# Performance work log

Measured on AMD Instinct MI355X. Metric: run time of the kernel, lower is better.

## Reference

```python
import jax, jax.numpy as jnp
import numpy as np

N, H, W, C = 4, 64, 64, 256
G, K = 8, 3
GC = C // G
P = K * K
PAD = 1
BN_EPS = 1e-3  # ultralytics Conv uses BatchNorm2d(eps=0.001)


def setup_inputs() -> dict:
    key = jax.random.key(0)
    ks = jax.random.split(key, 8)
    return {
        "x": jax.random.normal(ks[0], (N, H, W, C), jnp.float32),
        # depthwise conv weight (OIHW with I=1, feature_group_count=C)
        "dw_w": jax.random.normal(ks[1], (C, 1, K, K), jnp.float32) * 0.1,
        "bn_gamma": jnp.ones((C,), jnp.float32),
        "bn_beta": jnp.zeros((C,), jnp.float32),
        "bn_mean": jnp.zeros((C,), jnp.float32),
        "bn_var": jnp.ones((C,), jnp.float32),
        # offset/mask heads are zero-init in torch; use small random weights so
        # sampling locations are nontrivial but stay near the kernel grid
        "W_off": jax.random.normal(ks[2], (C, G * P * 2), jnp.float32) * 0.01,
        "b_off": jnp.zeros((G * P * 2,), jnp.float32),
        "W_mask": jax.random.normal(ks[3], (C, G * P), jnp.float32) * 0.01,
        "b_mask": jnp.zeros((G * P,), jnp.float32),
        "W_in": jax.random.normal(ks[4], (C, C), jnp.float32) / np.sqrt(C).astype(np.float32),
        "b_in": jnp.zeros((C,), jnp.float32),
        "W_out": jax.random.normal(ks[5], (C, C), jnp.float32) / np.sqrt(C).astype(np.float32),
        "b_out": jnp.zeros((C,), jnp.float32),
    }


def _grid_sample(img, grid):
    # img: (B, gc, Hi, Wi); grid: (B, L, P, 2) in [-1,1], (x,y) order.
    # Matches torch grid_sample(mode='bilinear', padding_mode='zeros', align_corners=False).
    B, gc, Hi, Wi = img.shape
    x = (grid[..., 0] + 1.0) * (Wi * 0.5) - 0.5
    y = (grid[..., 1] + 1.0) * (Hi * 0.5) - 0.5
    x0 = jnp.floor(x).astype(jnp.int32)
    y0 = jnp.floor(y).astype(jnp.int32)
    tx = x - x0
    ty = y - y0
    flat = img.reshape(B, gc, Hi * Wi)
    L, Pp = grid.shape[1], grid.shape[2]

    def tap(xi, yi, w):
        valid = (xi >= 0) & (xi < Wi) & (yi >= 0) & (yi < Hi)
        idx = jnp.clip(yi, 0, Hi - 1) * Wi + jnp.clip(xi, 0, Wi - 1)
        v = jnp.take_along_axis(flat, idx.reshape(B, 1, L * Pp), axis=2)
        v = v.reshape(B, gc, L, Pp)
        return v * (w * valid)[:, None]

    return (tap(x0, y0, (1 - tx) * (1 - ty))
            + tap(x0 + 1, y0, tx * (1 - ty))
            + tap(x0, y0 + 1, (1 - tx) * ty)
            + tap(x0 + 1, y0 + 1, tx * ty))


def _dcnv3_core(xp, offset, mask):
    # xp: (N,H,W,C) projected input; offset: (N,H,W,G*P*2); mask: (N,H,W,G*P)
    xpad = jnp.pad(xp, ((0, 0), (PAD, PAD), (PAD, PAD), (0, 0)))
    Hi, Wi = H + 2 * PAD, W + 2 * PAD
    # reference points on the padded grid, normalized to [0,1]
    start = (K - 1) // 2 + 0.5  # dilation=1, stride=1
    ref_y = (start + jnp.arange(H, dtype=jnp.float32)) / Hi
    ref_x = (start + jnp.arange(W, dtype=jnp.float32)) / Wi
    ref = jnp.stack(jnp.broadcast_arrays(ref_x[None, :], ref_y[:, None]), -1)  # (H,W,2) (x,y)
    # kernel dilation grid; torch meshgrid('ij') over (kw,kh) -> point p = iw*K + ih
    xv = jnp.arange(K, dtype=jnp.float32) - ((K - 1) // 2)
    gx, gy = jnp.meshgrid(xv / Wi, xv / Hi, indexing='ij')
    kgrid = jnp.stack([gx, gy], -1).reshape(P, 2)  # identical per group
    off = offset.reshape(N, H, W, G, P, 2) / jnp.array([Wi, Hi], jnp.float32)
    loc = ref[None, :, :, None, None, :] + kgrid[None, None, None, None] + off  # (N,H,W,G,P,2)
    sg = 2.0 * loc - 1.0
    # regroup channels-last input to (N*G, GC, Hi, Wi); channel c = g*GC + d
    img = xpad.reshape(N, Hi * Wi, G, GC).transpose(0, 2, 3, 1).reshape(N * G, GC, Hi, Wi)
    sgrid = sg.reshape(N, H * W, G, P, 2).transpose(0, 2, 1, 3, 4).reshape(N * G, H * W, P, 2)
    samp = _grid_sample(img, sgrid)  # (N*G, GC, L, P)
    m = mask.reshape(N, H * W, G, P).transpose(0, 2, 1, 3).reshape(N * G, 1, H * W, P)
    out = (samp * m).sum(-1)  # (N*G, GC, L)
    return out.reshape(N, C, H * W).transpose(0, 2, 1).reshape(N, H, W, C)


def reference(x, dw_w, bn_gamma, bn_beta, bn_mean, bn_var, W_off, b_off,
              W_mask, b_mask, W_in, b_in, W_out, b_out):
    x_proj = x @ W_in + b_in
    # depthwise 3x3 conv + BN (eval) + SiLU (ultralytics Conv)
    xc = x.transpose(0, 3, 1, 2)
    y = jax.lax.conv_general_dilated(
        xc, dw_w, (1, 1), ((PAD, PAD), (PAD, PAD)),
        feature_group_count=C, dimension_numbers=('NCHW', 'OIHW', 'NCHW'))
    scale = bn_gamma / jnp.sqrt(bn_var + BN_EPS)
    y = (y - bn_mean[None, :, None, None]) * scale[None, :, None, None] + bn_beta[None, :, None, None]
    y = y * jax.nn.sigmoid(y)
    x1 = y.transpose(0, 2, 3, 1)  # (N,H,W,C)
    offset = x1 @ W_off + b_off
    mlog = (x1 @ W_mask + b_mask).reshape(N, H, W, G, P)
    mask = jax.nn.softmax(mlog, axis=-1).reshape(N, H, W, G * P)
    out = _dcnv3_core(x_proj, offset, mask)
    return out @ W_out + b_out
```

## Files before the change

kernel.cpp:

```cpp
#include <hip/hip_runtime.h>
#include <math.h>

#define NPIX 16384
#define CC 256
#define OFFW 144
#define MSKW 72

typedef unsigned short ushortT;
typedef __attribute__((ext_vector_type(4))) float f32x4;
typedef __attribute__((ext_vector_type(8))) __bf16 bf16x8;
typedef __attribute__((ext_vector_type(8))) unsigned short u16x8;
typedef __attribute__((ext_vector_type(4))) unsigned int u32x4;

__device__ __forceinline__ float bf2f(ushortT u) {
    union { unsigned u; float f; } x; x.u = ((unsigned)u) << 16; return x.f;
}
__device__ __forceinline__ ushortT f2bf(float f) {
    __bf16 h = (__bf16)f;
    ushortT u;
    __builtin_memcpy(&u, &h, 2);
    return u;
}
__device__ __forceinline__ float bflo(unsigned u) { return __uint_as_float(u << 16); }
__device__ __forceinline__ float bfhi(unsigned u) { return __uint_as_float(u & 0xFFFF0000u); }

typedef __attribute__((address_space(3))) char lds_char;
typedef __attribute__((address_space(1))) char glb_char;
__device__ __forceinline__ void gload_lds16(const void* g, void* l) {
    __builtin_amdgcn_global_load_lds((const glb_char*)g, (lds_char*)l, 16, 0, 0);
}

__global__ __launch_bounds__(256) void k_wt(
    const float* __restrict__ W_in, const float* __restrict__ W_out,
    const float* __restrict__ W_off, const float* __restrict__ W_mask,
    const float* __restrict__ b_in, const float* __restrict__ b_out,
    const float* __restrict__ b_off, const float* __restrict__ b_mask,
    ushortT* __restrict__ Wt, float* __restrict__ biasb)
{
    const int idx = blockIdx.x * 256 + threadIdx.x;
    const int slot = idx >> 16;
    const int rem = idx & 65535;
    const int n = rem >> 8, k = rem & 255;
    float v;
    if (slot == 0)      v = W_in[k * 256 + n];
    else if (slot == 1) v = W_out[k * 256 + n];
    else {
        const int g = n >> 5, r = n & 31;
        if (r < 18)      v = W_off[k * OFFW + g * 18 + r];
        else if (r < 27) v = W_mask[k * MSKW + g * 9 + (r - 18)];
        else             v = 0.f;
    }
    Wt[idx] = f2bf(v);
    if (n == 0) {
        float b;
        if (slot == 0)      b = b_in[k];
        else if (slot == 1) b = b_out[k];
        else {
            const int g = k >> 5, r = k & 31;
            b = (r < 18) ? b_off[g * 18 + r] : (r < 27 ? b_mask[g * 9 + (r - 18)] : 0.f);
        }
        biasb[slot * 256 + k] = b;
    }
}

__global__ __launch_bounds__(512, 4) void k_fused_in(
    const float* __restrict__ x, const float* __restrict__ dw_w,
    const float* __restrict__ bn_gamma, const float* __restrict__ bn_beta,
    const float* __restrict__ bn_mean, const float* __restrict__ bn_var,
    const ushortT* __restrict__ Wt, const float* __restrict__ biasb,
    ushortT* __restrict__ xpb, ushortT* __restrict__ omb)
{
    __shared__ __align__(16) ushortT xA[32 * 256];
    __shared__ __align__(16) ushortT x1s[32 * 256];
    const int tid = threadIdx.x;
    const int b0 = blockIdx.x;
    const int lb = (b0 & 7) * 64 + (b0 >> 3);
    const int base = lb * 32;
    const int n = base >> 12, h = (base >> 6) & 63, bw0 = base & 63;

    const int lane = tid & 63, wave = tid >> 6;
    const int gemm = wave >> 2, wc = wave & 3;
    const ushortT* Bt = Wt + (gemm ? 2 * 65536 : 0);

    {
        const int c = tid & 255, half = tid >> 8;
        float wreg[9];
        #pragma unroll
        for (int k = 0; k < 9; ++k) wreg[k] = dw_w[c * 9 + k];
        const float scale = bn_gamma[c] * rsqrtf(bn_var[c] + 1e-3f);
        const float mean = bn_mean[c], beta = bn_beta[c];
        const bool hv0 = h >= 1, hv2 = h <= 62;
        const float* r0 = x + ((size_t)(n * 64 + h - 1) * 64) * 256 + c;
        const float* r1 = x + ((size_t)(n * 64 + h) * 64) * 256 + c;
        const float* r2 = x + ((size_t)(n * 64 + h + 1) * 64) * 256 + c;
        const int w0 = bw0 + half * 16;
        float a0, a1, a2, e0, e1, e2;
        if (w0 - 1 >= 0) {
            a0 = hv0 ? r0[(w0 - 1) * 256] : 0.f;
            a1 = r1[(w0 - 1) * 256];
            a2 = hv2 ? r2[(w0 - 1) * 256] : 0.f;
        } else { a0 = a1 = a2 = 0.f; }
        e0 = hv0 ? r0[w0 * 256] : 0.f;
        e1 = r1[w0 * 256];
        e2 = hv2 ? r2[w0 * 256] : 0.f;
        #pragma unroll
        for (int i = 0; i < 16; ++i) {
            const int w = w0 + i;
            float d0, d1, d2;
            if (w + 1 < 64) {
                d0 = hv0 ? r0[(w + 1) * 256] : 0.f;
                d1 = r1[(w + 1) * 256];
                d2 = hv2 ? r2[(w + 1) * 256] : 0.f;
            } else { d0 = d1 = d2 = 0.f; }
            const float accv = a0 * wreg[0] + e0 * wreg[1] + d0 * wreg[2]
                             + a1 * wreg[3] + e1 * wreg[4] + d1 * wreg[5]
                             + a2 * wreg[6] + e2 * wreg[7] + d2 * wreg[8];
            const float yv = (accv - mean) * scale + beta;
            const float s = yv * __builtin_amdgcn_rcpf(1.f + __expf(-yv));
            const int row = half * 16 + i;
            const int sb = (row * 512 + c * 2) ^ ((row & 15) << 4);
            *(ushortT*)((char*)x1s + sb) = f2bf(s);
            *(ushortT*)((char*)xA + sb) = f2bf(e1);
            a0 = e0; a1 = e1; a2 = e2;
            e0 = d0; e1 = d1; e2 = d2;
        }
    }

    bf16x8 bbp[4];
    #pragma unroll
    for (int nn = 0; nn < 4; ++nn) {
        const int ncol = wc * 64 + nn * 16 + (lane & 15);
        bbp[nn] = *(const bf16x8*)(Bt + (size_t)ncol * 256 + (lane >> 4) * 8);
    }
    __syncthreads();

    const ushortT* As = gemm ? x1s : xA;
    const float* bias = biasb + (gemm ? 512 : 0);
    ushortT* Cout = gemm ? omb : xpb;

    f32x4 acc[2][4];
    #pragma unroll
    for (int m = 0; m < 2; ++m)
        #pragma unroll
        for (int nn = 0; nn < 4; ++nn) acc[m][nn] = (f32x4){0.f, 0.f, 0.f, 0.f};

    #pragma unroll
    for (int k0 = 0; k0 < 256; k0 += 32) {
        bf16x8 af[2], bb[4];
        #pragma unroll
        for (int nn = 0; nn < 4; ++nn) bb[nn] = bbp[nn];
        if (k0 + 32 < 256) {
            #pragma unroll
            for (int nn = 0; nn < 4; ++nn) {
                const int ncol = wc * 64 + nn * 16 + (lane & 15);
                bbp[nn] = *(const bf16x8*)(Bt + (size_t)ncol * 256 + (k0 + 32) + (lane >> 4) * 8);
            }
        }
        #pragma unroll
        for (int m = 0; m < 2; ++m) {
            const int row = m * 16 + (lane & 15);
            af[m] = *(const bf16x8*)((const char*)As + row * 512 +
                     (((k0 + (lane >> 4) * 8) * 2) ^ ((row & 15) << 4)));
        }
        #pragma unroll
        for (int m = 0; m < 2; ++m)
            #pragma unroll
            for (int nn = 0; nn < 4; ++nn)
                acc[m][nn] = __builtin_amdgcn_mfma_f32_16x16x32_bf16(af[m], bb[nn], acc[m][nn], 0, 0, 0);
    }

    const int rbase = (lane >> 4) * 4, col16 = lane & 15;
    #pragma unroll
    for (int m = 0; m < 2; ++m) {
        #pragma unroll
        for (int nn = 0; nn < 4; ++nn) {
            const int col = wc * 64 + nn * 16 + col16;
            const float bj = bias[col];
            #pragma unroll
            for (int r = 0; r < 4; ++r) {
                const int row = m * 16 + rbase + r;
                Cout[(size_t)(base + row) * 256 + col] = f2bf(acc[m][nn][r] + bj);
            }
        }
    }
}

__global__ __launch_bounds__(256) void k_core(
    const ushortT* __restrict__ omb, const ushortT* __restrict__ xpb,
    ushortT* __restrict__ coreb)
{
    const int tid = threadIdx.x;
    const int b0 = blockIdx.x;
    const int lb = (b0 & 7) * 256 + (b0 >> 3);
    const int base = lb * 8;
    const int n = base >> 12, h = (base >> 6) & 63, w0 = base & 63;

    const int px = tid >> 5, g = (tid >> 2) & 7, o = tid & 3;

    const ushortT* omp = omb + (size_t)(base + px) * 256 + g * 32;
    const u32x4 L0 = *(const u32x4*)(omp);
    const u32x4 L1 = *(const u32x4*)(omp + 8);
    const u32x4 L2 = *(const u32x4*)(omp + 16);
    const u32x4 L3 = *(const u32x4*)(omp + 24);
    unsigned opair[9];
    #pragma unroll
    for (int p = 0; p < 4; ++p) { opair[p] = L0[p]; opair[4 + p] = L1[p]; }
    opair[8] = L2[0];
    float lg[9];
    lg[0] = bflo(L2[1]); lg[1] = bfhi(L2[1]);
    lg[2] = bflo(L2[2]); lg[3] = bfhi(L2[2]);
    lg[4] = bflo(L2[3]); lg[5] = bfhi(L2[3]);
    lg[6] = bflo(L3[0]); lg[7] = bfhi(L3[0]);
    lg[8] = bflo(L3[1]);
    float mx = -1e30f;
    #pragma unroll
    for (int p = 0; p < 9; ++p) mx = fmaxf(mx, lg[p]);
    float sum = 0.f;
    #pragma unroll
    for (int p = 0; p < 9; ++p) sum += __expf(lg[p] - mx);
    const float inv = __builtin_amdgcn_rcpf(sum);

    const ushortT* xn = xpb + (size_t)n * (4096 * 256) + g * 32 + o * 8;
    float acc[8];
    #pragma unroll
    for (int j = 0; j < 8; ++j) acc[j] = 0.f;

    #pragma unroll
    for (int p = 0; p < 9; ++p) {
        const float m = __expf(lg[p] - mx) * inv;
        const float ox = bflo(opair[p]), oy = bfhi(opair[p]);
        const float pxc = (float)(w0 + px + p / 3) + ox;
        const float pyc = (float)(h + p % 3) + oy;
        const float xf = floorf(pxc), yf = floorf(pyc);
        const float tx = pxc - xf, ty = pyc - yf;
        const int x0 = (int)xf - 1, y0 = (int)yf - 1;
        const int x1 = x0 + 1, y1 = y0 + 1;
        const float wx0 = ((unsigned)x0 < 64u) ? (1.f - tx) : 0.f;
        const float wx1 = ((unsigned)x1 < 64u) ? tx : 0.f;
        const float wy0 = ((unsigned)y0 < 64u) ? (1.f - ty) : 0.f;
        const float wy1 = ((unsigned)y1 < 64u) ? ty : 0.f;
        const int cx0 = min(max(x0, 0), 63), cx1 = min(max(x1, 0), 63);
        const int cy0 = min(max(y0, 0), 63), cy1 = min(max(y1, 0), 63);
        const int o00 = (cy0 * 64 + cx0) * 256;
        const int o10 = (cy0 * 64 + cx1) * 256;
        const int o01 = (cy1 * 64 + cx0) * 256;
        const int o11 = (cy1 * 64 + cx1) * 256;
        const float w00 = m * wx0 * wy0, w10 = m * wx1 * wy0;
        const float w01 = m * wx0 * wy1, w11 = m * wx1 * wy1;
        const u32x4 A = *(const u32x4*)(xn + o00);
        const u32x4 B = *(const u32x4*)(xn + o10);
        const u32x4 C = *(const u32x4*)(xn + o01);
        const u32x4 D = *(const u32x4*)(xn + o11);
        #pragma unroll
        for (int i = 0; i < 4; ++i) {
            acc[2 * i]     += w00 * bflo(A[i]) + w10 * bflo(B[i])
                            + w01 * bflo(C[i]) + w11 * bflo(D[i]);
            acc[2 * i + 1] += w00 * bfhi(A[i]) + w10 * bfhi(B[i])
                            + w01 * bfhi(C[i]) + w11 * bfhi(D[i]);
        }
    }
    u16x8 cv;
    #pragma unroll
    for (int j = 0; j < 8; ++j) cv[j] = f2bf(acc[j]);
    *(u16x8*)(coreb + (size_t)(base + px) * 256 + g * 32 + o * 8) = cv;
}

__global__ __launch_bounds__(512) void k_gemm_out(
    const ushortT* __restrict__ A, const ushortT* __restrict__ Bt,
    const float* __restrict__ bias, float* __restrict__ out)
{
    __shared__ __align__(16) ushortT As[32 * 256];
    const int tid = threadIdx.x;
    const int m0 = blockIdx.x * 32;
    const int lane = tid & 63, wave = tid >> 6;

    #pragma unroll
    for (int it = 0; it < 2; ++it) {
        const int i = it * 512 + tid;
        const int row = i >> 5, ch = i & 31;
        const int sch = ch ^ (row & 15);
        gload_lds16(A + (size_t)(m0 + row) * 256 + sch * 8, (char*)As + i * 16);
    }
    bf16x8 bbp[2];
    #pragma unroll
    for (int nn = 0; nn < 2; ++nn) {
        const int ncol = wave * 32 + nn * 16 + (lane & 15);
        bbp[nn] = *(const bf16x8*)(Bt + (size_t)ncol * 256 + (lane >> 4) * 8);
    }
    asm volatile("s_waitcnt vmcnt(0)");
    __syncthreads();

    f32x4 acc[2][2];
    #pragma unroll
    for (int m = 0; m < 2; ++m)
        #pragma unroll
        for (int nn = 0; nn < 2; ++nn) acc[m][nn] = (f32x4){0.f, 0.f, 0.f, 0.f};

    #pragma unroll
    for (int k0 = 0; k0 < 256; k0 += 32) {
        bf16x8 af[2], bb[2];
        #pragma unroll
        for (int nn = 0; nn < 2; ++nn) bb[nn] = bbp[nn];
        if (k0 + 32 < 256) {
            #pragma unroll
            for (int nn = 0; nn < 2; ++nn) {
                const int ncol = wave * 32 + nn * 16 + (lane & 15);
                bbp[nn] = *(const bf16x8*)(Bt + (size_t)ncol * 256 + (k0 + 32) + (lane >> 4) * 8);
            }
        }
        #pragma unroll
        for (int m = 0; m < 2; ++m) {
            const int row = m * 16 + (lane & 15);
            af[m] = *(const bf16x8*)((const char*)As + row * 512 +
                     (((k0 + (lane >> 4) * 8) * 2) ^ ((row & 15) << 4)));
        }
        #pragma unroll
        for (int m = 0; m < 2; ++m)
            #pragma unroll
            for (int nn = 0; nn < 2; ++nn)
                acc[m][nn] = __builtin_amdgcn_mfma_f32_16x16x32_bf16(af[m], bb[nn], acc[m][nn], 0, 0, 0);
    }

    const int rbase = (lane >> 4) * 4, col16 = lane & 15;
    #pragma unroll
    for (int m = 0; m < 2; ++m) {
        #pragma unroll
        for (int nn = 0; nn < 2; ++nn) {
            const int col = wave * 32 + nn * 16 + col16;
            const float bj = bias[col];
            #pragma unroll
            for (int r = 0; r < 4; ++r) {
                const int row = m0 + m * 16 + rbase + r;
                out[(size_t)row * 256 + col] = acc[m][nn][r] + bj;
            }
        }
    }
}

extern "C" void kernel_launch(void* const* d_in, const int* in_sizes, int n_in,
                              void* d_out, int out_size, void* d_ws, size_t ws_size,
                              hipStream_t stream) {
    const float* x        = (const float*)d_in[0];
    const float* dw_w     = (const float*)d_in[1];
    const float* bn_gamma = (const float*)d_in[2];
    const float* bn_beta  = (const float*)d_in[3];
    const float* bn_mean  = (const float*)d_in[4];
    const float* bn_var   = (const float*)d_in[5];
    const float* W_off    = (const float*)d_in[6];
    const float* b_off    = (const float*)d_in[7];
    const float* W_mask   = (const float*)d_in[8];
    const float* b_mask   = (const float*)d_in[9];
    const float* W_in     = (const float*)d_in[10];
    const float* b_in     = (const float*)d_in[11];
    const float* W_out    = (const float*)d_in[12];
    const float* b_out    = (const float*)d_in[13];
    float* out = (float*)d_out;

    char* w = (char*)d_ws;
    ushortT* Wt    = (ushortT*)w;
    float* biasb   = (float*)(w + 393216);
    ushortT* xpb   = (ushortT*)(w + 396288);
    ushortT* omb   = (ushortT*)(w + 396288 + 8388608);
    ushortT* coreb = (ushortT*)(w + 396288 + 2 * 8388608);

    hipLaunchKernelGGL(k_wt, dim3(768), dim3(256), 0, stream,
                       W_in, W_out, W_off, W_mask, b_in, b_out, b_off, b_mask, Wt, biasb);
    hipLaunchKernelGGL(k_fused_in, dim3(512), dim3(512), 0, stream,
                       x, dw_w, bn_gamma, bn_beta, bn_mean, bn_var, Wt, biasb, xpb, omb);
    hipLaunchKernelGGL(k_core, dim3(2048), dim3(256), 0, stream,
                       omb, xpb, coreb);
    hipLaunchKernelGGL(k_gemm_out, dim3(NPIX / 32), dim3(512), 0, stream,
                       coreb, Wt + 65536, biasb + 256, out);
}
```

Measured before the change: 63.88 us.

## Fuse deformable sampling core with output projection GEMM via LDS

Merges the bilinear-sampling core kernel and the output-projection MFMA GEMM into one kernel. Each 512-thread block samples 32 pixels, with each thread now handling 16 channels, and writes the bf16 result into a swizzled LDS tile that feeds the GEMM directly. This removes the global round trip of the intermediate core tensor and one kernel launch. In exchange there are fewer, larger blocks (512 instead of 2048 core blocks) with more registers per thread, which may reduce latency hiding for the gather loads.

```diff
diff --git a/kernel.cpp b/kernel.cpp
--- a/kernel.cpp
+++ b/kernel.cpp
@@ -23,12 +23,6 @@
 }
 __device__ __forceinline__ float bflo(unsigned u) { return __uint_as_float(u << 16); }
 __device__ __forceinline__ float bfhi(unsigned u) { return __uint_as_float(u & 0xFFFF0000u); }
-
-typedef __attribute__((address_space(3))) char lds_char;
-typedef __attribute__((address_space(1))) char glb_char;
-__device__ __forceinline__ void gload_lds16(const void* g, void* l) {
-    __builtin_amdgcn_global_load_lds((const glb_char*)g, (lds_char*)l, 16, 0, 0);
-}
 
 __global__ __launch_bounds__(256) void k_wt(
     const float* __restrict__ W_in, const float* __restrict__ W_out,
@@ -185,116 +179,117 @@
     }
 }
 
-__global__ __launch_bounds__(256) void k_core(
+__global__ __launch_bounds__(512) void k_core_out(
     const ushortT* __restrict__ omb, const ushortT* __restrict__ xpb,
-    ushortT* __restrict__ coreb)
+    const ushortT* __restrict__ Wt1, const float* __restrict__ bias1,
+    float* __restrict__ out)
 {
+    __shared__ __align__(16) ushortT core[32 * 256];
     const int tid = threadIdx.x;
     const int b0 = blockIdx.x;
-    const int lb = (b0 & 7) * 256 + (b0 >> 3);
-    const int base = lb * 8;
+    const int lb = (b0 & 7) * 64 + (b0 >> 3);
+    const int base = lb * 32;
     const int n = base >> 12, h = (base >> 6) & 63, w0 = base & 63;
 
-    const int px = tid >> 5, g = (tid >> 2) & 7, o = tid & 3;
-
-    const ushortT* omp = omb + (size_t)(base + px) * 256 + g * 32;
-    const u32x4 L0 = *(const u32x4*)(omp);
-    const u32x4 L1 = *(const u32x4*)(omp + 8);
-    const u32x4 L2 = *(const u32x4*)(omp + 16);
-    const u32x4 L3 = *(const u32x4*)(omp + 24);
-    unsigned opair[9];
-    #pragma unroll
-    for (int p = 0; p < 4; ++p) { opair[p] = L0[p]; opair[4 + p] = L1[p]; }
-    opair[8] = L2[0];
-    float lg[9];
-    lg[0] = bflo(L2[1]); lg[1] = bfhi(L2[1]);
-    lg[2] = bflo(L2[2]); lg[3] = bfhi(L2[2]);
-    lg[4] = bflo(L2[3]); lg[5] = bfhi(L2[3]);
-    lg[6] = bflo(L3[0]); lg[7] = bfhi(L3[0]);
-    lg[8] = bflo(L3[1]);
-    float mx = -1e30f;
-    #pragma unroll
-    for (int p = 0; p < 9; ++p) mx = fmaxf(mx, lg[p]);
-    float sum = 0.f;
-    #pragma unroll
-    for (int p = 0; p < 9; ++p) sum += __expf(lg[p] - mx);
-    const float inv = __builtin_amdgcn_rcpf(sum);
-
-    const ushortT* xn = xpb + (size_t)n * (4096 * 256) + g * 32 + o * 8;
-    float acc[8];
-    #pragma unroll
-    for (int j = 0; j < 8; ++j) acc[j] = 0.f;
-
-    #pragma unroll
-    for (int p = 0; p < 9; ++p) {
-        const float m = __expf(lg[p] - mx) * inv;
-        const float ox = bflo(opair[p]), oy = bfhi(opair[p]);
-        const float pxc = (float)(w0 + px + p / 3) + ox;
-        const float pyc = (float)(h + p % 3) + oy;
-        const float xf = floorf(pxc), yf = floorf(pyc);
-        const float tx = pxc - xf, ty = pyc - yf;
-        const int x0 = (int)xf - 1, y0 = (int)yf - 1;
-        const int x1 = x0 + 1, y1 = y0 + 1;
-        const float wx0 = ((unsigned)x0 < 64u) ? (1.f - tx) : 0.f;
-        const float wx1 = ((unsigned)x1 < 64u) ? tx : 0.f;
-        const float wy0 = ((unsigned)y0 < 64u) ? (1.f - ty) : 0.f;
-        const float wy1 = ((unsigned)y1 < 64u) ? ty : 0.f;
-        const int cx0 = min(max(x0, 0), 63), cx1 = min(max(x1, 0), 63);
-        const int cy0 = min(max(y0, 0), 63), cy1 = min(max(y1, 0), 63);
-        const int o00 = (cy0 * 64 + cx0) * 256;
-        const int o10 = (cy0 * 64 + cx1) * 256;
-        const int o01 = (cy1 * 64 + cx0) * 256;
-        const int o11 = (cy1 * 64 + cx1) * 256;
-        const float w00 = m * wx0 * wy0, w10 = m * wx1 * wy0;
-        const float w01 = m * wx0 * wy1, w11 = m * wx1 * wy1;
-        const u32x4 A = *(const u32x4*)(xn + o00);
-        const u32x4 B = *(const u32x4*)(xn + o10);
-        const u32x4 C = *(const u32x4*)(xn + o01);
-        const u32x4 D = *(const u32x4*)(xn + o11);
-        #pragma unroll
-        for (int i = 0; i < 4; ++i) {
-            acc[2 * i]     += w00 * bflo(A[i]) + w10 * bflo(B[i])
-                            + w01 * bflo(C[i]) + w11 * bflo(D[i]);
-            acc[2 * i + 1] += w00 * bfhi(A[i]) + w10 * bfhi(B[i])
-                            + w01 * bfhi(C[i]) + w11 * bfhi(D[i]);
-        }
-    }
-    u16x8 cv;
-    #pragma unroll
-    for (int j = 0; j < 8; ++j) cv[j] = f2bf(acc[j]);
-    *(u16x8*)(coreb + (size_t)(base + px) * 256 + g * 32 + o * 8) = cv;
-}
-
-__global__ __launch_bounds__(512) void k_gemm_out(
-    const ushortT* __restrict__ A, const ushortT* __restrict__ Bt,
-    const float* __restrict__ bias, float* __restrict__ out)
-{
-    __shared__ __align__(16) ushortT As[32 * 256];
-    const int tid = threadIdx.x;
-    const int m0 = blockIdx.x * 32;
     const int lane = tid & 63, wave = tid >> 6;
 
-    #pragma unroll
-    for (int it = 0; it < 2; ++it) {
-        const int i = it * 512 + tid;
-        const int row = i >> 5, ch = i & 31;
-        const int sch = ch ^ (row & 15);
-        gload_lds16(A + (size_t)(m0 + row) * 256 + sch * 8, (char*)As + i * 16);
-    }
+    {
+        const int px = tid >> 4, s = tid & 15;
+        const int g = s >> 1, half = s & 1;
+        const int c0 = g * 32 + half * 16;
+
+        const ushortT* omp = omb + (size_t)(base + px) * 256 + g * 32;
+        const u32x4 L0 = *(const u32x4*)(omp);
+        const u32x4 L1 = *(const u32x4*)(omp + 8);
+        const u32x4 L2 = *(const u32x4*)(omp + 16);
+        const u32x4 L3 = *(const u32x4*)(omp + 24);
+        unsigned opair[9];
+        #pragma unroll
+        for (int p = 0; p < 4; ++p) { opair[p] = L0[p]; opair[4 + p] = L1[p]; }
+        opair[8] = L2[0];
+        float lg[9];
+        lg[0] = bflo(L2[1]); lg[1] = bfhi(L2[1]);
+        lg[2] = bflo(L2[2]); lg[3] = bfhi(L2[2]);
+        lg[4] = bflo(L2[3]); lg[5] = bfhi(L2[3]);
+        lg[6] = bflo(L3[0]); lg[7] = bfhi(L3[0]);
+        lg[8] = bflo(L3[1]);
+        float mx = -1e30f;
+        #pragma unroll
+        for (int p = 0; p < 9; ++p) mx = fmaxf(mx, lg[p]);
+        float sum = 0.f;
+        #pragma unroll
+        for (int p = 0; p < 9; ++p) sum += __expf(lg[p] - mx);
+        const float inv = __builtin_amdgcn_rcpf(sum);
+
+        const ushortT* xn = xpb + (size_t)n * (4096 * 256) + c0;
+        float acc[16];
+        #pragma unroll
+        for (int j = 0; j < 16; ++j) acc[j] = 0.f;
+
+        #pragma unroll
+        for (int p = 0; p < 9; ++p) {
+            const float m = __expf(lg[p] - mx) * inv;
+            const float ox = bflo(opair[p]), oy = bfhi(opair[p]);
+            const float pxc = (float)(w0 + px + p / 3) + ox;
+            const float pyc = (float)(h + p % 3) + oy;
+            const float xf = floorf(pxc), yf = floorf(pyc);
+            const float tx = pxc - xf, ty = pyc - yf;
+            const int x0 = (int)xf - 1, y0 = (int)yf - 1;
+            const int x1 = x0 + 1, y1 = y0 + 1;
+            const float wx0 = ((unsigned)x0 < 64u) ? (1.f - tx) : 0.f;
+            const float wx1 = ((unsigned)x1 < 64u) ? tx : 0.f;
+            const float wy0 = ((unsigned)y0 < 64u) ? (1.f - ty) : 0.f;
+            const float wy1 = ((unsigned)y1 < 64u) ? ty : 0.f;
+            const int cx0 = min(max(x0, 0), 63), cx1 = min(max(x1, 0), 63);
+            const int cy0 = min(max(y0, 0), 63), cy1 = min(max(y1, 0), 63);
+            const int o00 = (cy0 * 64 + cx0) * 256;
+            const int o10 = (cy0 * 64 + cx1) * 256;
+            const int o01 = (cy1 * 64 + cx0) * 256;
+            const int o11 = (cy1 * 64 + cx1) * 256;
+            const float w00 = m * wx0 * wy0, w10 = m * wx1 * wy0;
+            const float w01 = m * wx0 * wy1, w11 = m * wx1 * wy1;
+            const u32x4 A0 = *(const u32x4*)(xn + o00);
+            const u32x4 A1 = *(const u32x4*)(xn + o00 + 8);
+            const u32x4 B0 = *(const u32x4*)(xn + o10);
+            const u32x4 B1 = *(const u32x4*)(xn + o10 + 8);
+            const u32x4 C0 = *(const u32x4*)(xn + o01);
+            const u32x4 C1 = *(const u32x4*)(xn + o01 + 8);
+            const u32x4 D0 = *(const u32x4*)(xn + o11);
+            const u32x4 D1 = *(const u32x4*)(xn + o11 + 8);
+            #pragma unroll
+            for (int i = 0; i < 4; ++i) {
+                acc[2 * i]     += w00 * bflo(A0[i]) + w10 * bflo(B0[i])
+                                + w01 * bflo(C0[i]) + w11 * bflo(D0[i]);
+                acc[2 * i + 1] += w00 * bfhi(A0[i]) + w10 * bfhi(B0[i])
+                                + w01 * bfhi(C0[i]) + w11 * bfhi(D0[i]);
+                acc[8 + 2 * i]     += w00 * bflo(A1[i]) + w10 * bflo(B1[i])
+                                    + w01 * bflo(C1[i]) + w11 * bflo(D1[i]);
+                acc[8 + 2 * i + 1] += w00 * bfhi(A1[i]) + w10 * bfhi(B1[i])
+                                    + w01 * bfhi(C1[i]) + w11 * bfhi(D1[i]);
+            }
+        }
+        u16x8 cv0, cv1;
+        #pragma unroll
+        for (int j = 0; j < 8; ++j) { cv0[j] = f2bf(acc[j]); cv1[j] = f2bf(acc[8 + j]); }
+        const int sb0 = (px * 512 + c0 * 2) ^ ((px & 15) << 4);
+        const int sb1 = (px * 512 + c0 * 2 + 16) ^ ((px & 15) << 4);
+        *(u16x8*)((char*)core + sb0) = cv0;
+        *(u16x8*)((char*)core + sb1) = cv1;
+    }
+
     bf16x8 bbp[2];
     #pragma unroll
     for (int nn = 0; nn < 2; ++nn) {
         const int ncol = wave * 32 + nn * 16 + (lane & 15);
-        bbp[nn] = *(const bf16x8*)(Bt + (size_t)ncol * 256 + (lane >> 4) * 8);
-    }
-    asm volatile("s_waitcnt vmcnt(0)");
+        bbp[nn] = *(const bf16x8*)(Wt1 + (size_t)ncol * 256 + (lane >> 4) * 8);
+    }
     __syncthreads();
 
-    f32x4 acc[2][2];
+    f32x4 acc2[2][2];
     #pragma unroll
     for (int m = 0; m < 2; ++m)
         #pragma unroll
-        for (int nn = 0; nn < 2; ++nn) acc[m][nn] = (f32x4){0.f, 0.f, 0.f, 0.f};
+        for (int nn = 0; nn < 2; ++nn) acc2[m][nn] = (f32x4){0.f, 0.f, 0.f, 0.f};
 
     #pragma unroll
     for (int k0 = 0; k0 < 256; k0 += 32) {
@@ -305,20 +300,20 @@
             #pragma unroll
             for (int nn = 0; nn < 2; ++nn) {
                 const int ncol = wave * 32 + nn * 16 + (lane & 15);
-                bbp[nn] = *(const bf16x8*)(Bt + (size_t)ncol * 256 + (k0 + 32) + (lane >> 4) * 8);
+                bbp[nn] = *(const bf16x8*)(Wt1 + (size_t)ncol * 256 + (k0 + 32) + (lane >> 4) * 8);
             }
         }
         #pragma unroll
         for (int m = 0; m < 2; ++m) {
             const int row = m * 16 + (lane & 15);
-            af[m] = *(const bf16x8*)((const char*)As + row * 512 +
+            af[m] = *(const bf16x8*)((const char*)core + row * 512 +
                      (((k0 + (lane >> 4) * 8) * 2) ^ ((row & 15) << 4)));
         }
         #pragma unroll
         for (int m = 0; m < 2; ++m)
             #pragma unroll
             for (int nn = 0; nn < 2; ++nn)
-                acc[m][nn] = __builtin_amdgcn_mfma_f32_16x16x32_bf16(af[m], bb[nn], acc[m][nn], 0, 0, 0);
+                acc2[m][nn] = __builtin_amdgcn_mfma_f32_16x16x32_bf16(af[m], bb[nn], acc2[m][nn], 0, 0, 0);
     }
 
     const int rbase = (lane >> 4) * 4, col16 = lane & 15;
@@ -327,11 +322,11 @@
         #pragma unroll
         for (int nn = 0; nn < 2; ++nn) {
             const int col = wave * 32 + nn * 16 + col16;
-            const float bj = bias[col];
+            const float bj = bias1[col];
             #pragma unroll
             for (int r = 0; r < 4; ++r) {
-                const int row = m0 + m * 16 + rbase + r;
-                out[(size_t)row * 256 + col] = acc[m][nn][r] + bj;
+                const int row = base + m * 16 + rbase + r;
+                out[(size_t)row * 256 + col] = acc2[m][nn][r] + bj;
             }
         }
     }
@@ -361,14 +356,11 @@
     float* biasb   = (float*)(w + 393216);
     ushortT* xpb   = (ushortT*)(w + 396288);
     ushortT* omb   = (ushortT*)(w + 396288 + 8388608);
-    ushortT* coreb = (ushortT*)(w + 396288 + 2 * 8388608);
 
     hipLaunchKernelGGL(k_wt, dim3(768), dim3(256), 0, stream,
                        W_in, W_out, W_off, W_mask, b_in, b_out, b_off, b_mask, Wt, biasb);
     hipLaunchKernelGGL(k_fused_in, dim3(512), dim3(512), 0, stream,
                        x, dw_w, bn_gamma, bn_beta, bn_mean, bn_var, Wt, biasb, xpb, omb);
-    hipLaunchKernelGGL(k_core, dim3(2048), dim3(256), 0, stream,
-                       omb, xpb, coreb);
-    hipLaunchKernelGGL(k_gemm_out, dim3(NPIX / 32), dim3(512), 0, stream,
-                       coreb, Wt + 65536, biasb + 256, out);
-}
+    hipLaunchKernelGGL(k_core_out, dim3(512), dim3(512), 0, stream,
+                       omb, xpb, Wt + 65536, biasb + 256, out);
+}
```

Result: slower. 114.1 us (+78.5%).
